# Performance work log

Hardware: AMD Instinct MI355X
Metric: run time of the kernel (lower is better)

## Reference

```python
import jax, jax.numpy as jnp
from jax import lax
import numpy as np

B, C_IN, IMG = 128, 3, 64
NH, D, K = 128, 256, 1024
BETA = 0.1        # beta buffer initialized to beta_start
BA_ITERS = 5
EPS = 1e-10


def _conv(x, w, b, stride, pad):
    y = lax.conv_general_dilated(x, w, (stride, stride), ((pad, pad), (pad, pad)),
                                 dimension_numbers=("NCHW", "OIHW", "NCHW"))
    return y + b[None, :, None, None]


def _convT(x, w, b):
    # PyTorch ConvTranspose2d(k=4, s=2, p=1); w: [Cin, Cout, 4, 4]
    wt = jnp.flip(w, (2, 3)).transpose(1, 0, 2, 3)  # -> [Cout, Cin, 4, 4]
    y = lax.conv_general_dilated(x, wt, (1, 1), ((2, 2), (2, 2)),
                                 lhs_dilation=(2, 2),
                                 dimension_numbers=("NCHW", "OIHW", "NCHW"))
    return y + b[None, :, None, None]


def _res(x, w1, b1, w2, b2):
    h = jax.nn.relu(_conv(x, w1, b1, 1, 1))
    h = _conv(h, w2, b2, 1, 1)
    return jax.nn.relu(h + x)


def setup_inputs() -> dict:
    key = jax.random.key(0)
    ks = iter(jax.random.split(key, 40))

    def w(shape):
        fan_in = int(np.prod(shape[1:]))
        return jax.random.normal(next(ks), shape, jnp.float32) / np.float32(np.sqrt(fan_in))

    z = lambda n: jnp.zeros((n,), jnp.float32)
    inp = {"x": jax.random.normal(next(ks), (B, C_IN, IMG, IMG), jnp.float32)}
    inp.update(
        ew1=w((NH, 3, 4, 4)), eb1=z(NH),
        ew2=w((2 * NH, NH, 4, 4)), eb2=z(2 * NH),
        ew3=w((D, 2 * NH, 3, 3)), eb3=z(D),
        er1aw=w((D, D, 3, 3)), er1ab=z(D), er1bw=w((D, D, 3, 3)), er1bb=z(D),
        er2aw=w((D, D, 3, 3)), er2ab=z(D), er2bw=w((D, D, 3, 3)), er2bb=z(D),
        codebook=jax.random.uniform(next(ks), (K, D), jnp.float32, -1.0 / K, 1.0 / K),
        pi=jnp.full((K,), 1.0 / K, jnp.float32),
        dr1aw=w((D, D, 3, 3)), dr1ab=z(D), dr1bw=w((D, D, 3, 3)), dr1bb=z(D),
        dr2aw=w((D, D, 3, 3)), dr2ab=z(D), dr2bw=w((D, D, 3, 3)), dr2bb=z(D),
        dw1=w((2 * NH, D, 3, 3)), db1=z(2 * NH),
        dwt2=w((2 * NH, NH, 4, 4)), dbt2=z(NH),
        dwt3=w((NH, 3, 4, 4)), dbt3=z(3),
    )
    return inp


def reference(x, ew1, eb1, ew2, eb2, ew3, eb3,
              er1aw, er1ab, er1bw, er1bb, er2aw, er2ab, er2bw, er2bb,
              codebook, pi,
              dr1aw, dr1ab, dr1bw, dr1bb, dr2aw, dr2ab, dr2bw, dr2bb,
              dw1, db1, dwt2, dbt2, dwt3, dbt3):
    # ---- encoder: [B,3,H,W] -> [B,D,H/4,W/4] ----
    h = jax.nn.relu(_conv(x, ew1, eb1, 2, 1))
    h = jax.nn.relu(_conv(h, ew2, eb2, 2, 1))
    h = jax.nn.relu(_conv(h, ew3, eb3, 1, 1))
    h = _res(h, er1aw, er1ab, er1bw, er1bb)
    z = _res(h, er2aw, er2ab, er2bw, er2bb)

    Bn, Dn, Hl, Wl = z.shape
    zf = z.transpose(0, 2, 3, 1).reshape(-1, Dn)  # [N, D]

    # squared euclidean distances [N, K]
    d = (jnp.sum(zf * zf, axis=1, keepdims=True)
         + jnp.sum(codebook * codebook, axis=1)
         - 2.0 * (zf @ codebook.T))

    # ---- Blahut-Arimoto iterations ----
    Q = pi
    for _ in range(BA_ITERS):
        logits = jnp.log(jnp.clip(Q, EPS)) - BETA * d  # [N, K]
        P = jax.nn.softmax(logits, axis=1)
        Q = jnp.clip(jnp.mean(P, axis=0), EPS)

    zq_soft = P @ codebook                              # [N, D]
    idx = jnp.argmax(P, axis=1)

    commit = 0.25 * jnp.mean((zf - lax.stop_gradient(zq_soft)) ** 2)
    cb_loss = jnp.mean((zq_soft - lax.stop_gradient(zf)) ** 2)
    ent = -jnp.sum(Q * jnp.log(jnp.clip(Q, EPS)))
    ent_loss = -0.01 * ent

    zq_hard = codebook[idx]
    zq = zq_soft + lax.stop_gradient(zq_hard - zq_soft)  # straight-through
    zq = zq.reshape(Bn, Hl, Wl, Dn).transpose(0, 3, 1, 2)

    # ---- decoder ----
    h = _res(zq, dr1aw, dr1ab, dr1bw, dr1bb)
    h = _res(h, dr2aw, dr2ab, dr2bw, dr2bb)
    h = jax.nn.relu(_conv(h, dw1, db1, 1, 1))
    h = jax.nn.relu(_convT(h, dwt2, dbt2))
    x_recon = _convT(h, dwt3, dbt3)
    return x_recon, commit, cb_loss, ent_loss
```

## Files before the change

### kernel.cpp

```cpp
#include <hip/hip_runtime.h>
#include <math.h>

#define NB   128
#define DC   256
#define SP   256
#define NROW 32768
#define KCB  1024
#define BETA_F 0.1f
#define EPSQ 1e-10f

typedef __attribute__((ext_vector_type(8))) short s16x8;
typedef __attribute__((ext_vector_type(4))) short s16x4;
typedef __attribute__((ext_vector_type(4))) float f32x4;

__device__ __forceinline__ short f2bf(float f) {
  unsigned u = __builtin_bit_cast(unsigned, f);
  unsigned r = (u + 0x7FFFu + ((u >> 16) & 1u)) >> 16;
  return (short)r;
}
__device__ __forceinline__ float bf2f(short s) {
  unsigned u = ((unsigned)(unsigned short)s) << 16;
  return __builtin_bit_cast(float, u);
}
__device__ __forceinline__ unsigned pack2(float a, float b) {
  return (unsigned)(unsigned short)f2bf(a) | ((unsigned)(unsigned short)f2bf(b) << 16);
}

__global__ void init0_kernel(short* __restrict__ zerob, unsigned* __restrict__ ticket)
{
  if (threadIdx.x < 8) zerob[threadIdx.x] = 0;
  if (threadIdx.x == 0) *ticket = 0u;
}

__global__ void w3t10_kernel(
    const float* __restrict__ w0, const float* __restrict__ w1,
    const float* __restrict__ w2, const float* __restrict__ w3,
    const float* __restrict__ w4, const float* __restrict__ w5,
    const float* __restrict__ w6, const float* __restrict__ w7,
    const float* __restrict__ w8, const float* __restrict__ w9,
    short* __restrict__ o)
{
  const float* ws[10] = {w0, w1, w2, w3, w4, w5, w6, w7, w8, w9};
  const float* w = ws[blockIdx.y];
  const int i = blockIdx.x * 256 + threadIdx.x;
  const int ci = i & 255, co = (i >> 8) & 255, j = i >> 16;
  o[(size_t)blockIdx.y * 589824 + i] = f2bf(w[((size_t)(co * 256 + ci)) * 9 + j]);
}
__global__ void w2t_kernel(const float* __restrict__ w, short* __restrict__ o)
{
  const int i = blockIdx.x * 256 + threadIdx.x;
  const int ci = i & 127, co = (i >> 7) & 255, j = i >> 15;
  o[i] = f2bf(w[((size_t)(co * 128 + ci)) * 16 + j]);
}
__global__ void wtt2_kernel(const float* __restrict__ w, short* __restrict__ o)
{
  const int i = blockIdx.x * 256 + threadIdx.x;
  const int ci = i & 255, co = (i >> 8) & 127, j = (i >> 15) & 3, p = i >> 17;
  const int po = p >> 1, pq = p & 1, a = j >> 1, b2 = j & 1;
  const int kh = (1 - po) + 2 * a, kw = (1 - pq) + 2 * b2;
  o[i] = f2bf(w[((size_t)(ci * 128 + co)) * 16 + kh * 4 + kw]);
}
__global__ void cbbf_kernel(const float* __restrict__ cb, short* __restrict__ o)
{
  const int i = blockIdx.x * 256 + threadIdx.x;
  o[i] = f2bf(cb[i]);
}
__global__ void cbt_kernel(const float* __restrict__ cb, short* __restrict__ o)
{
  const int i = blockIdx.x * 256 + threadIdx.x;
  const int d = i >> 10, k = i & 1023;
  o[i] = f2bf(cb[(size_t)k * 256 + d]);
}

__global__ __launch_bounds__(256) void conv1_kernel(
    const float* __restrict__ x, const float* __restrict__ w,
    const float* __restrict__ bias, short* __restrict__ out)
{
  __shared__ float li[3][34][34];
  const int tid = threadIdx.x;
  const int tile = blockIdx.x;
  const int b = blockIdx.y;
  const int qy = tile >> 1, qx = tile & 1;
  const int ihlo = qy * 32 - 1, iwlo = qx * 32 - 1;
  for (int ci = 0; ci < 3; ++ci)
    for (int s = tid; s < 1156; s += 256) {
      const int r = s / 34, c = s - r * 34;
      const int ih = ihlo + r, iw = iwlo + c;
      float v = 0.f;
      if ((unsigned)ih < 64u && (unsigned)iw < 64u)
        v = x[((size_t)(b * 3 + ci) * 64 + ih) * 64 + iw];
      li[ci][r][c] = v;
    }
  __syncthreads();

  const int wv = tid >> 6, l = tid & 63;
  const int co0 = 2 * l, co1 = 2 * l + 1;
  float w0[48], w1[48];
#pragma unroll
  for (int j = 0; j < 48; ++j) {
    w0[j] = w[(size_t)co0 * 48 + j];
    w1[j] = w[(size_t)co1 * 48 + j];
  }
  const float b0 = bias[co0], b1 = bias[co1];

  for (int pass = 0; pass < 64; ++pass) {
    const int pix = pass * 4 + wv;
    const int py = pix >> 4, px = pix & 15;
    float s0 = b0, s1 = b1;
#pragma unroll
    for (int ci = 0; ci < 3; ++ci)
#pragma unroll
      for (int kh = 0; kh < 4; ++kh)
#pragma unroll
        for (int kw = 0; kw < 4; ++kw) {
          const int j = ci * 16 + kh * 4 + kw;
          const float v = li[ci][2 * py + kh][2 * px + kw];
          s0 = fmaf(v, w0[j], s0);
          s1 = fmaf(v, w1[j], s1);
        }
    s0 = fmaxf(s0, 0.f);
    s1 = fmaxf(s1, 0.f);
    const int oh = qy * 16 + py, ow = qx * 16 + px;
    ((unsigned*)(out + ((size_t)b * 1024 + oh * 32 + ow) * 128))[l] = pack2(s0, s1);
  }
}

template<int MODE, int KIT, int AK, int KPN, int TS>
__global__ __launch_bounds__(256) void igemm_kernel(
    const short* __restrict__ Abuf, const short* __restrict__ Bw,
    const float* __restrict__ bias, const short* __restrict__ res,
    short* __restrict__ outb, float* __restrict__ outf32,
    float* __restrict__ sacc, const short* __restrict__ zerob)
{
  __shared__ __align__(16) short Alds[4][8192];
  __shared__ float red[4];
  const int tid = threadIdx.x;
  const int wv = tid >> 6, l = tid & 63;
  const int wm = wv >> 1, wn = wv & 1;
  const int lcol = l & 15, lk = l >> 4;
  const int m0 = blockIdx.x * 128;

  int ncol0 = 0, po = 0, pq = 0;
  const short* Bp = Bw;
  if constexpr (MODE == 3) {
    po = blockIdx.y >> 1; pq = blockIdx.y & 1;
    Bp += (size_t)blockIdx.y * 131072;
  } else {
    ncol0 = blockIdx.y * 128;
    Bp += (size_t)ncol0 * KPN;
  }

  const int cpos = l & 3;
  const int rl_[2] = { (wv * 2) * 16 + (l >> 2), (wv * 2 + 1) * 16 + (l >> 2) };
  const int cc_[2] = { cpos ^ ((rl_[0] >> 1) & 3), cpos ^ ((rl_[1] >> 1) & 3) };

  f32x4 acc[4][4];
#pragma unroll
  for (int i = 0; i < 4; ++i)
#pragma unroll
    for (int j = 0; j < 4; ++j) acc[i][j] = (f32x4){0.f, 0.f, 0.f, 0.f};

  const int aoff_base = lcol * 32 + ((lk ^ ((lcol >> 1) & 3)) * 8);

  auto STAGE = [&](int it, int bufc) {
    int jj, kk;
    if constexpr (MODE == 0 || MODE == 3) { jj = it >> 3; kk = it & 7; }
    else if constexpr (MODE == 2)         { jj = it >> 2; kk = it & 3; }
    else                                  { jj = 0; kk = it; }
    const int choff = kk * 32;
    (void)jj;
#pragma unroll
    for (int q = 0; q < 2; ++q) {
      const int rl = rl_[q], cc = cc_[q];
      const int m = m0 + rl;
      const short* srcA;
      if constexpr (MODE == 0) {
        const int q3 = jj / 3;
        const int ih = ((m >> 4) & 15) + q3 - 1, iw = (m & 15) + (jj - q3 * 3) - 1;
        const bool v = ((unsigned)ih < 16u) & ((unsigned)iw < 16u);
        srcA = v ? Abuf + (size_t)((m & ~255) + ih * 16 + iw) * AK + choff + cc * 8 : zerob;
      } else if constexpr (MODE == 2) {
        const int ih = 2 * ((m >> 4) & 15) + (jj >> 2) - 1, iw = 2 * (m & 15) + (jj & 3) - 1;
        const bool v = ((unsigned)ih < 32u) & ((unsigned)iw < 32u);
        srcA = v ? Abuf + (size_t)((m >> 8) * 1024 + ih * 32 + iw) * AK + choff + cc * 8 : zerob;
      } else if constexpr (MODE == 3) {
        const int ih = ((m >> 4) & 15) + po - (jj >> 1), iw = (m & 15) + pq - (jj & 1);
        const bool v = ((unsigned)ih < 16u) & ((unsigned)iw < 16u);
        srcA = v ? Abuf + (size_t)((m & ~255) + ih * 16 + iw) * AK + choff + cc * 8 : zerob;
      } else {
        srcA = Abuf + (size_t)m * AK + choff + cc * 8;
      }
      __builtin_amdgcn_global_load_lds(
          (const __attribute__((address_space(1))) void*)srcA,
          (__attribute__((address_space(3))) void*)(&Alds[bufc][(wv * 2 + q) * 512]),
          16, 0, 0);
      const short* srcB = Bp + (size_t)jj * TS + (size_t)rl * KPN + choff + cc * 8;
      __builtin_amdgcn_global_load_lds(
          (const __attribute__((address_space(1))) void*)srcB,
          (__attribute__((address_space(3))) void*)(&Alds[bufc][4096 + (wv * 2 + q) * 512]),
          16, 0, 0);
    }
  };

  auto COMPUTE = [&](int bufc) {
    s16x8 a[4], b[4];
#pragma unroll
    for (int ms = 0; ms < 4; ++ms)
      a[ms] = *(const s16x8*)&Alds[bufc][wm * 2048 + ms * 512 + aoff_base];
#pragma unroll
    for (int ns = 0; ns < 4; ++ns)
      b[ns] = *(const s16x8*)&Alds[bufc][4096 + wn * 2048 + ns * 512 + aoff_base];
#pragma unroll
    for (int ms = 0; ms < 4; ++ms)
#pragma unroll
      for (int ns = 0; ns < 4; ++ns)
        acc[ms][ns] = __builtin_amdgcn_mfma_f32_16x16x32_bf16(a[ms], b[ns], acc[ms][ns], 0, 0, 0);
  };

  STAGE(0, 0);
  STAGE(1, 1);
  STAGE(2, 2);
  int buf = 0, nbuf = 3;
#pragma unroll 1
  for (int it = 0; it < KIT; ++it) {
    if (it + 2 < KIT) {
      asm volatile("s_waitcnt vmcnt(8)" ::: "memory");
    } else if (it + 1 < KIT) {
      asm volatile("s_waitcnt vmcnt(4)" ::: "memory");
    } else {
      asm volatile("s_waitcnt vmcnt(0)" ::: "memory");
    }
    __builtin_amdgcn_s_barrier();
    if (it + 3 < KIT) STAGE(it + 3, nbuf);
    __builtin_amdgcn_s_setprio(1);
    COMPUTE(buf);
    __builtin_amdgcn_s_setprio(0);
    buf = (buf + 1) & 3;
    nbuf = (nbuf + 1) & 3;
  }

  const int r4 = lk * 4;
  float ls = 0.f;
#pragma unroll
  for (int ms = 0; ms < 4; ++ms) {
#pragma unroll
    for (int ns = 0; ns < 4; ++ns) {
      const int n_l = wn * 64 + ns * 16 + lcol;
      const int n_g = ncol0 + n_l;
#pragma unroll
      for (int e = 0; e < 4; ++e) {
        const int m = m0 + wm * 64 + ms * 16 + r4 + e;
        if constexpr (MODE == 4) {
          const float val = bias[n_g] - 2.f * acc[ms][ns][e];
          outb[(size_t)m * 1024 + n_g] = f2bf(val);
        } else if constexpr (MODE == 5) {
          const float d = acc[ms][ns][e] - outf32[(size_t)m * 256 + n_g];
          ls = fmaf(d, d, ls);
        } else if constexpr (MODE == 3) {
          const float val = fmaxf(acc[ms][ns][e] + bias[n_l], 0.f);
          const int orow = (m & ~255) * 4 + (2 * ((m >> 4) & 15) + po) * 32 + (2 * (m & 15) + pq);
          outb[(size_t)orow * 128 + n_l] = f2bf(val);
        } else {
          float val = acc[ms][ns][e] + bias[n_g];
          if (res) val += bf2f(res[(size_t)m * 256 + n_g]);
          val = fmaxf(val, 0.f);
          outb[(size_t)m * 256 + n_g] = f2bf(val);
          if (outf32) outf32[(size_t)m * 256 + n_g] = val;
        }
      }
    }
  }
  if constexpr (MODE == 5) {
#pragma unroll
    for (int o = 32; o > 0; o >>= 1) ls += __shfl_xor(ls, o);
    if (l == 0) red[wv] = ls;
    __syncthreads();
    if (tid == 0) atomicAdd(sacc, red[0] + red[1] + red[2] + red[3]);
  }
}

__global__ __launch_bounds__(256) void rownorm_kernel(
    const float* __restrict__ a, float* __restrict__ nrm, int rows)
{
  const int wv = threadIdx.x >> 6, lane = threadIdx.x & 63;
  const int r = blockIdx.x * 4 + wv;
  if (r >= rows) return;
  const float* p = a + (size_t)r * DC;
  float s = 0.f;
#pragma unroll
  for (int i = 0; i < 4; ++i) { float v = p[lane + 64 * i]; s = fmaf(v, v, s); }
#pragma unroll
  for (int o = 32; o > 0; o >>= 1) s += __shfl_xor(s, o);
  if (lane == 0) nrm[r] = s;
}

__global__ void initq_kernel(const float* __restrict__ pi, float* __restrict__ logq,
                             float* __restrict__ Sacc)
{
  const int k = blockIdx.x * 256 + threadIdx.x;
  logq[k] = logf(fmaxf(pi[k], EPSQ));
  if (k == 0) *Sacc = 0.f;
}

__global__ __launch_bounds__(256) void ba2_kernel(
    uint4* __restrict__ DV, const float* __restrict__ logq,
    float* __restrict__ part, int* __restrict__ idxout, int storeP)
{
  __shared__ float qp[4][1024];
  const int tid = threadIdx.x;
  const int wv = tid >> 6, lane = tid & 63;

  float lq[16];
  {
    const float4* lq4 = (const float4*)logq;
#pragma unroll
    for (int h = 0; h < 2; ++h) {
      const float4 a = lq4[h * 128 + 2 * lane];
      const float4 b = lq4[h * 128 + 2 * lane + 1];
      lq[h * 8 + 0] = a.x; lq[h * 8 + 1] = a.y; lq[h * 8 + 2] = a.z; lq[h * 8 + 3] = a.w;
      lq[h * 8 + 4] = b.x; lq[h * 8 + 5] = b.y; lq[h * 8 + 6] = b.z; lq[h * 8 + 7] = b.w;
    }
  }

  float qacc[16];
#pragma unroll
  for (int j = 0; j < 16; ++j) qacc[j] = 0.f;

  const int n0 = blockIdx.x * 16;
  for (int rr = 0; rr < 4; ++rr) {
    const int n = n0 + wv * 4 + rr;
    uint4* rowp = DV + (size_t)n * 128;
    uint4 w[2];
    w[0] = rowp[lane];
    w[1] = rowp[64 + lane];
    float lv[16];
    float mx = -1e30f;
#pragma unroll
    for (int h = 0; h < 2; ++h) {
      const unsigned* u = (const unsigned*)&w[h];
#pragma unroll
      for (int p = 0; p < 4; ++p) {
        lv[h * 8 + 2 * p]     = lq[h * 8 + 2 * p]     - BETA_F * bf2f((short)(u[p] & 0xFFFFu));
        lv[h * 8 + 2 * p + 1] = lq[h * 8 + 2 * p + 1] - BETA_F * bf2f((short)(u[p] >> 16));
      }
    }
#pragma unroll
    for (int j = 0; j < 16; ++j) mx = fmaxf(mx, lv[j]);
#pragma unroll
    for (int o = 32; o > 0; o >>= 1) mx = fmaxf(mx, __shfl_xor(mx, o));
    float e[16];
    float s = 0.f;
#pragma unroll
    for (int j = 0; j < 16; ++j) { e[j] = __expf(lv[j] - mx); s += e[j]; }
#pragma unroll
    for (int o = 32; o > 0; o >>= 1) s += __shfl_xor(s, o);
    const float inv = 1.f / s;
#pragma unroll
    for (int j = 0; j < 16; ++j) qacc[j] += e[j] * inv;

    if (storeP) {
#pragma unroll
      for (int h = 0; h < 2; ++h) {
        unsigned* u = (unsigned*)&w[h];
#pragma unroll
        for (int p = 0; p < 4; ++p)
          u[p] = pack2(e[h * 8 + 2 * p] * inv, e[h * 8 + 2 * p + 1] * inv);
      }
      rowp[lane] = w[0];
      rowp[64 + lane] = w[1];
      float bv = lv[0]; int bi = 8 * lane;
#pragma unroll
      for (int h = 0; h < 2; ++h)
#pragma unroll
        for (int j = 0; j < 8; ++j) {
          const int k = h * 512 + 8 * lane + j;
          const float v = lv[h * 8 + j];
          if (v > bv || (v == bv && k < bi)) { bv = v; bi = k; }
        }
#pragma unroll
      for (int o = 32; o > 0; o >>= 1) {
        const float ov = __shfl_xor(bv, o);
        const int oi = __shfl_xor(bi, o);
        if (ov > bv || (ov == bv && oi < bi)) { bv = ov; bi = oi; }
      }
      if (lane == 0) idxout[n] = bi;
    }
  }
  __syncthreads();
#pragma unroll
  for (int h = 0; h < 2; ++h)
#pragma unroll
    for (int j = 0; j < 8; ++j)
      qp[wv][h * 512 + 8 * lane + j] = qacc[h * 8 + j];
  __syncthreads();
  for (int k = tid; k < 1024; k += 256) {
    part[(size_t)blockIdx.x * 1024 + k] = qp[0][k] + qp[1][k] + qp[2][k] + qp[3][k];
  }
}

__global__ __launch_bounds__(256) void qredf_kernel(
    const float* __restrict__ part, float* __restrict__ part2,
    float* __restrict__ qsum, float* __restrict__ logq, unsigned* __restrict__ ticket)
{
  const int b = blockIdx.x;
  const int tid = threadIdx.x;
  const float* p = part + (size_t)b * 32 * 1024;
#pragma unroll
  for (int j = 0; j < 4; ++j) {
    const int k = tid + j * 256;
    float s = 0.f;
#pragma unroll
    for (int r = 0; r < 32; ++r) s += p[(size_t)r * 1024 + k];
    part2[(size_t)b * 1024 + k] = s;
  }
  __threadfence();
  __shared__ unsigned lastv;
  if (tid == 0) lastv = atomicAdd(ticket, 1u);
  __syncthreads();
  if (lastv == 63u) {
    __threadfence();
#pragma unroll
    for (int j = 0; j < 4; ++j) {
      const int k = tid + j * 256;
      float s = 0.f;
#pragma unroll
      for (int r = 0; r < 64; ++r) s += part2[(size_t)r * 1024 + k];
      qsum[k] = s;
      logq[k] = logf(fmaxf(s * (1.f / 32768.f), EPSQ));
    }
    if (tid == 0) *ticket = 0u;
  }
}

__global__ __launch_bounds__(1024) void entsc_kernel(
    const float* __restrict__ qsum, const float* __restrict__ S, float* __restrict__ out3)
{
  const int k = threadIdx.x;
  const float q = fmaxf(qsum[k] * (1.f / 32768.f), EPSQ);
  float v = q * logf(q);
#pragma unroll
  for (int o = 32; o > 0; o >>= 1) v += __shfl_xor(v, o);
  __shared__ float red[16];
  const int wv = k >> 6, lane = k & 63;
  if (lane == 0) red[wv] = v;
  __syncthreads();
  if (k == 0) {
    float s = 0.f;
    for (int i = 0; i < 16; ++i) s += red[i];
    out3[2] = 0.01f * s;
    const float sa = *S;
    out3[0] = 0.25f * sa / 8388608.f;
    out3[1] = sa / 8388608.f;
  }
}

__global__ void gather16_kernel(const int* __restrict__ idx, const short* __restrict__ cbb,
                                short* __restrict__ out)
{
  const int t = blockIdx.x * 256 + threadIdx.x;
  const int m = t >> 6, d4 = (t & 63) * 4;
  *(s16x4*)(out + (size_t)m * 256 + d4) = *(const s16x4*)(cbb + (size_t)idx[m] * 256 + d4);
}

__global__ __launch_bounds__(256) void convt3_kernel(
    const short* __restrict__ in, const float* __restrict__ w,
    const float* __restrict__ bias, float* __restrict__ out)
{
  __shared__ __align__(16) short li[100 * 128];
  __shared__ float lw[6144];
  const int tid = threadIdx.x;
  const int tile = blockIdx.x;
  const int b = blockIdx.y;
  const int ty0 = (tile >> 2) * 16, tx0 = (tile & 3) * 16;
  const int iy0 = (tile >> 2) * 8 - 1, ix0 = (tile & 3) * 8 - 1;
  for (int s = tid; s < 1600; s += 256) {
    const int pix = s >> 4, ch = s & 15;
    const int r = pix / 10, c = pix - r * 10;
    const int ih = iy0 + r, iw = ix0 + c;
    s16x8 v = {0, 0, 0, 0, 0, 0, 0, 0};
    if ((unsigned)ih < 32u && (unsigned)iw < 32u)
      v = *(const s16x8*)(in + ((size_t)b * 1024 + ih * 32 + iw) * 128 + ch * 8);
    const int slot = ch ^ (pix & 15);
    *(s16x8*)&li[pix * 128 + slot * 8] = v;
  }
  for (int s = tid; s < 6144; s += 256) lw[s] = w[s];
  __syncthreads();
  const int ty = tid >> 4, tx = tid & 15;
  const int oh2 = ty0 + ty, ow2 = tx0 + tx;
  const int kh0 = (oh2 + 1) & 1, kw0 = (ow2 + 1) & 1;
  const int ih0 = (oh2 + 1 - kh0) >> 1, iw0 = (ow2 + 1 - kw0) >> 1;
  const int rl0 = ih0 - iy0, cl0 = iw0 - ix0;
  const int p00 = rl0 * 10 + cl0, p01 = p00 - 1, p10 = p00 - 10, p11 = p00 - 11;
  const int wi00 = kh0 * 4 + kw0, wi01 = wi00 + 2, wi10 = wi00 + 8, wi11 = wi00 + 10;
  float acc0 = 0.f, acc1 = 0.f, acc2 = 0.f;
  for (int ch = 0; ch < 16; ++ch) {
    const s16x8 v00 = *(const s16x8*)&li[p00 * 128 + (ch ^ (p00 & 15)) * 8];
    const s16x8 v01 = *(const s16x8*)&li[p01 * 128 + (ch ^ (p01 & 15)) * 8];
    const s16x8 v10 = *(const s16x8*)&li[p10 * 128 + (ch ^ (p10 & 15)) * 8];
    const s16x8 v11 = *(const s16x8*)&li[p11 * 128 + (ch ^ (p11 & 15)) * 8];
#pragma unroll
    for (int e = 0; e < 8; ++e) {
      const int ci = ch * 8 + e;
      const float* wr = &lw[ci * 48];
      const float f00 = bf2f(v00[e]), f01 = bf2f(v01[e]);
      const float f10 = bf2f(v10[e]), f11 = bf2f(v11[e]);
      acc0 = fmaf(wr[wi00], f00, fmaf(wr[wi01], f01, fmaf(wr[wi10], f10, fmaf(wr[wi11], f11, acc0))));
      acc1 = fmaf(wr[16 + wi00], f00, fmaf(wr[16 + wi01], f01, fmaf(wr[16 + wi10], f10, fmaf(wr[16 + wi11], f11, acc1))));
      acc2 = fmaf(wr[32 + wi00], f00, fmaf(wr[32 + wi01], f01, fmaf(wr[32 + wi10], f10, fmaf(wr[32 + wi11], f11, acc2))));
    }
  }
  const size_t ob = ((size_t)(b * 3) * 64 + oh2) * 64 + ow2;
  out[ob] = acc0 + bias[0];
  out[ob + 4096] = acc1 + bias[1];
  out[ob + 8192] = acc2 + bias[2];
}

extern "C" void kernel_launch(void* const* d_in, const int* in_sizes, int n_in,
                              void* d_out, int out_size, void* d_ws, size_t ws_size,
                              hipStream_t stream)
{
  const float* x     = (const float*)d_in[0];
  const float* ew1   = (const float*)d_in[1];
  const float* eb1   = (const float*)d_in[2];
  const float* ew2   = (const float*)d_in[3];
  const float* eb2   = (const float*)d_in[4];
  const float* ew3   = (const float*)d_in[5];
  const float* eb3   = (const float*)d_in[6];
  const float* er1aw = (const float*)d_in[7];
  const float* er1ab = (const float*)d_in[8];
  const float* er1bw = (const float*)d_in[9];
  const float* er1bb = (const float*)d_in[10];
  const float* er2aw = (const float*)d_in[11];
  const float* er2ab = (const float*)d_in[12];
  const float* er2bw = (const float*)d_in[13];
  const float* er2bb = (const float*)d_in[14];
  const float* cb    = (const float*)d_in[15];
  const float* pi    = (const float*)d_in[16];
  const float* dr1aw = (const float*)d_in[17];
  const float* dr1ab = (const float*)d_in[18];
  const float* dr1bw = (const float*)d_in[19];
  const float* dr1bb = (const float*)d_in[20];
  const float* dr2aw = (const float*)d_in[21];
  const float* dr2ab = (const float*)d_in[22];
  const float* dr2bw = (const float*)d_in[23];
  const float* dr2bb = (const float*)d_in[24];
  const float* dw1   = (const float*)d_in[25];
  const float* db1   = (const float*)d_in[26];
  const float* dwt2  = (const float*)d_in[27];
  const float* dbt2  = (const float*)d_in[28];
  const float* dwt3  = (const float*)d_in[29];
  const float* dbt3  = (const float*)d_in[30];

  float* outf = (float*)d_out;

  char* W = (char*)d_ws;
  short* BIGA  = (short*)W;
  float* ZF32  = (float*)W;
  short* DV    = (short*)(W + 33554432);
  short* X0    = (short*)(W + 100663296);
  short* X1    = (short*)(W + 117440512);
  short* X2    = (short*)(W + 134217728);
  short* WT2   = (short*)(W + 152174592);
  short* WTT2  = (short*)(W + 153223168);
  short* CBB   = (short*)(W + 154271744);
  short* CBT   = (short*)(W + 154796032);
  float* cn    = (float*)(W + 155320320);
  float* qsum  = (float*)(W + 155324416);
  float* logq  = (float*)(W + 155328512);
  int*   idx   = (int*)(W + 155332608);
  float* Sacc  = (float*)(W + 155463680);
  short* zerob = (short*)(W + 155463696);
  unsigned* ticket = (unsigned*)(W + 155463712);
  float* PART  = (float*)(W + 160000000);
  float* PART2 = (float*)(W + 168388608);
  short* WT3S  = (short*)(W + 168650752);

  const dim3 blk(256);
  #define WTSLAB(i) (WT3S + (size_t)(i) * 589824)
  #define IG3(A_, Wi_, B_, R_, O_, F_) \
    igemm_kernel<0,72,256,256,65536><<<dim3(256, 2), blk, 0, stream>>>( \
        A_, WTSLAB(Wi_), B_, R_, O_, F_, nullptr, zerob)

  init0_kernel<<<dim3(1), dim3(64), 0, stream>>>(zerob, ticket);
  w3t10_kernel<<<dim3(2304, 10), blk, 0, stream>>>(
      ew3, er1aw, er1bw, er2aw, er2bw, dr1aw, dr1bw, dr2aw, dr2bw, dw1, WT3S);

  conv1_kernel<<<dim3(4, NB), blk, 0, stream>>>(x, ew1, eb1, BIGA);
  w2t_kernel<<<dim3(2048), blk, 0, stream>>>(ew2, WT2);
  igemm_kernel<2,64,128,128,32768><<<dim3(256, 2), blk, 0, stream>>>(
      BIGA, WT2, eb2, nullptr, X0, nullptr, nullptr, zerob);
  IG3(X0, 0, eb3, nullptr, X1, nullptr);
  IG3(X1, 1, er1ab, nullptr, X2, nullptr);
  IG3(X2, 2, er1bb, X1, X0, nullptr);
  IG3(X0, 3, er2ab, nullptr, X1, nullptr);
  IG3(X1, 4, er2bb, X0, X2, ZF32);

  rownorm_kernel<<<dim3(KCB / 4), blk, 0, stream>>>(cb, cn, KCB);
  cbbf_kernel<<<dim3(1024), blk, 0, stream>>>(cb, CBB);
  cbt_kernel<<<dim3(1024), blk, 0, stream>>>(cb, CBT);
  initq_kernel<<<dim3(4), blk, 0, stream>>>(pi, logq, Sacc);
  igemm_kernel<4,8,256,256,0><<<dim3(256, 8), blk, 0, stream>>>(
      X2, CBB, cn, nullptr, DV, nullptr, nullptr, zerob);
  for (int i = 0; i < 5; ++i) {
    ba2_kernel<<<dim3(NROW / 16), blk, 0, stream>>>(
        (uint4*)DV, logq, PART, idx, (i == 4) ? 1 : 0);
    qredf_kernel<<<dim3(64), blk, 0, stream>>>(PART, PART2, qsum, logq, ticket);
  }
  igemm_kernel<5,32,1024,1024,0><<<dim3(256, 2), blk, 0, stream>>>(
      DV, CBT, nullptr, nullptr, nullptr, ZF32, Sacc, zerob);
  entsc_kernel<<<dim3(1), dim3(1024), 0, stream>>>(qsum, Sacc, outf + 1572864);
  gather16_kernel<<<dim3(8192), blk, 0, stream>>>(idx, CBB, X0);

  IG3(X0, 5, dr1ab, nullptr, X1, nullptr);
  IG3(X1, 6, dr1bb, X0, X2, nullptr);
  IG3(X2, 7, dr2ab, nullptr, X0, nullptr);
  IG3(X0, 8, dr2bb, X2, X1, nullptr);
  IG3(X1, 9, db1, nullptr, X0, nullptr);
  wtt2_kernel<<<dim3(2048), blk, 0, stream>>>(dwt2, WTT2);
  igemm_kernel<3,32,256,256,32768><<<dim3(256, 4), blk, 0, stream>>>(
      X0, WTT2, dbt2, nullptr, BIGA, nullptr, nullptr, zerob);
  convt3_kernel<<<dim3(16, NB), blk, 0, stream>>>(BIGA, dwt3, dbt3, outf);
  #undef IG3
  #undef WTSLAB
}
```

Baseline: 949.0 us.

## Use 512-thread 128x256 tile GEMM kernel for non-transpose convolutions

Adds an 8-wave igemm variant whose block computes a 128x256 output tile, so each A tile staged in LDS is reused across all 256 output columns instead of being reloaded by two 128-column blocks. The grid halves in the N dimension and LDS per block grows to 96KB across four buffers. The old kernel is reduced to the transposed-conv mode only. This cuts redundant A-operand global traffic, but lowers the number of blocks and may reduce occupancy.

```diff
diff --git a/kernel.cpp b/kernel.cpp
--- a/kernel.cpp
+++ b/kernel.cpp
@@ -126,6 +126,152 @@
 }
 
 template<int MODE, int KIT, int AK, int KPN, int TS>
+__global__ __launch_bounds__(512) void igemm8_kernel(
+    const short* __restrict__ Abuf, const short* __restrict__ Bw,
+    const float* __restrict__ bias, const short* __restrict__ res,
+    short* __restrict__ outb, float* __restrict__ outf32,
+    float* __restrict__ sacc, const short* __restrict__ zerob)
+{
+  __shared__ __align__(16) short Alds[4][12288];
+  __shared__ float red[8];
+  const int tid = threadIdx.x;
+  const int wv = tid >> 6, l = tid & 63;
+  const int wm = wv >> 2, wn = wv & 3;
+  const int lcol = l & 15, lk = l >> 4;
+  const int m0 = blockIdx.x * 128;
+
+  const int ncol0 = blockIdx.y * 256;
+  const short* Bp = Bw + (size_t)ncol0 * KPN;
+
+  const int rlA = wv * 16 + (l >> 2);
+  const int ccA = (l & 3) ^ ((rlA >> 1) & 3);
+  const int colB_[2] = { wv * 32 + (l >> 2), wv * 32 + 16 + (l >> 2) };
+  const int ccB_[2] = { (l & 3) ^ ((colB_[0] >> 1) & 3), (l & 3) ^ ((colB_[1] >> 1) & 3) };
+
+  f32x4 acc[4][4];
+#pragma unroll
+  for (int i = 0; i < 4; ++i)
+#pragma unroll
+    for (int j = 0; j < 4; ++j) acc[i][j] = (f32x4){0.f, 0.f, 0.f, 0.f};
+
+  const int aoff_base = lcol * 32 + ((lk ^ ((lcol >> 1) & 3)) * 8);
+
+  auto STAGE = [&](int it, int bufc) {
+    int jj, kk;
+    if constexpr (MODE == 0)      { jj = it >> 3; kk = it & 7; }
+    else if constexpr (MODE == 2) { jj = it >> 2; kk = it & 3; }
+    else                          { jj = 0; kk = it; }
+    const int choff = kk * 32;
+    (void)jj;
+    {
+      const int m = m0 + rlA;
+      const short* srcA;
+      if constexpr (MODE == 0) {
+        const int q3 = jj / 3;
+        const int ih = ((m >> 4) & 15) + q3 - 1, iw = (m & 15) + (jj - q3 * 3) - 1;
+        const bool v = ((unsigned)ih < 16u) & ((unsigned)iw < 16u);
+        srcA = v ? Abuf + (size_t)((m & ~255) + ih * 16 + iw) * AK + choff + ccA * 8 : zerob;
+      } else if constexpr (MODE == 2) {
+        const int ih = 2 * ((m >> 4) & 15) + (jj >> 2) - 1, iw = 2 * (m & 15) + (jj & 3) - 1;
+        const bool v = ((unsigned)ih < 32u) & ((unsigned)iw < 32u);
+        srcA = v ? Abuf + (size_t)((m >> 8) * 1024 + ih * 32 + iw) * AK + choff + ccA * 8 : zerob;
+      } else {
+        srcA = Abuf + (size_t)m * AK + choff + ccA * 8;
+      }
+      __builtin_amdgcn_global_load_lds(
+          (const __attribute__((address_space(1))) void*)srcA,
+          (__attribute__((address_space(3))) void*)(&Alds[bufc][wv * 512]),
+          16, 0, 0);
+    }
+#pragma unroll
+    for (int q = 0; q < 2; ++q) {
+      const short* srcB = Bp + (size_t)jj * TS + (size_t)colB_[q] * KPN + choff + ccB_[q] * 8;
+      __builtin_amdgcn_global_load_lds(
+          (const __attribute__((address_space(1))) void*)srcB,
+          (__attribute__((address_space(3))) void*)(&Alds[bufc][4096 + wv * 1024 + q * 512]),
+          16, 0, 0);
+    }
+  };
+
+  auto COMPUTE = [&](int bufc) {
+    s16x8 a[4], b[4];
+#pragma unroll
+    for (int ms = 0; ms < 4; ++ms)
+      a[ms] = *(const s16x8*)&Alds[bufc][wm * 2048 + ms * 512 + aoff_base];
+#pragma unroll
+    for (int ns = 0; ns < 4; ++ns)
+      b[ns] = *(const s16x8*)&Alds[bufc][4096 + wn * 2048 + ns * 512 + aoff_base];
+#pragma unroll
+    for (int ms = 0; ms < 4; ++ms)
+#pragma unroll
+      for (int ns = 0; ns < 4; ++ns)
+        acc[ms][ns] = __builtin_amdgcn_mfma_f32_16x16x32_bf16(a[ms], b[ns], acc[ms][ns], 0, 0, 0);
+  };
+
+  STAGE(0, 0);
+  STAGE(1, 1);
+  STAGE(2, 2);
+  int buf = 0, nbuf = 3;
+#pragma unroll 1
+  for (int it = 0; it < KIT; ++it) {
+    if (it + 2 < KIT) {
+      asm volatile("s_waitcnt vmcnt(6)" ::: "memory");
+    } else if (it + 1 < KIT) {
+      asm volatile("s_waitcnt vmcnt(3)" ::: "memory");
+    } else {
+      asm volatile("s_waitcnt vmcnt(0)" ::: "memory");
+    }
+    __builtin_amdgcn_s_barrier();
+    if (it + 3 < KIT) STAGE(it + 3, nbuf);
+    __builtin_amdgcn_s_setprio(1);
+    COMPUTE(buf);
+    __builtin_amdgcn_s_setprio(0);
+    buf = (buf + 1) & 3;
+    nbuf = (nbuf + 1) & 3;
+  }
+
+  const int r4 = lk * 4;
+  float ls = 0.f;
+#pragma unroll
+  for (int ms = 0; ms < 4; ++ms) {
+#pragma unroll
+    for (int ns = 0; ns < 4; ++ns) {
+      const int n_l = wn * 64 + ns * 16 + lcol;
+      const int n_g = ncol0 + n_l;
+#pragma unroll
+      for (int e = 0; e < 4; ++e) {
+        const int m = m0 + wm * 64 + ms * 16 + r4 + e;
+        if constexpr (MODE == 4) {
+          const float val = bias[n_g] - 2.f * acc[ms][ns][e];
+          outb[(size_t)m * 1024 + n_g] = f2bf(val);
+        } else if constexpr (MODE == 5) {
+          const float d = acc[ms][ns][e] - outf32[(size_t)m * 256 + n_g];
+          ls = fmaf(d, d, ls);
+        } else {
+          float val = acc[ms][ns][e] + bias[n_g];
+          if (res) val += bf2f(res[(size_t)m * 256 + n_g]);
+          val = fmaxf(val, 0.f);
+          outb[(size_t)m * 256 + n_g] = f2bf(val);
+          if (outf32) outf32[(size_t)m * 256 + n_g] = val;
+        }
+      }
+    }
+  }
+  if constexpr (MODE == 5) {
+#pragma unroll
+    for (int o = 32; o > 0; o >>= 1) ls += __shfl_xor(ls, o);
+    if (l == 0) red[wv] = ls;
+    __syncthreads();
+    if (tid == 0) {
+      float s = 0.f;
+#pragma unroll
+      for (int i = 0; i < 8; ++i) s += red[i];
+      atomicAdd(sacc, s);
+    }
+  }
+}
+
+template<int MODE, int KIT, int AK, int KPN, int TS>
 __global__ __launch_bounds__(256) void igemm_kernel(
     const short* __restrict__ Abuf, const short* __restrict__ Bw,
     const float* __restrict__ bias, const short* __restrict__ res,
@@ -133,22 +279,14 @@
     float* __restrict__ sacc, const short* __restrict__ zerob)
 {
   __shared__ __align__(16) short Alds[4][8192];
-  __shared__ float red[4];
   const int tid = threadIdx.x;
   const int wv = tid >> 6, l = tid & 63;
   const int wm = wv >> 1, wn = wv & 1;
   const int lcol = l & 15, lk = l >> 4;
   const int m0 = blockIdx.x * 128;
 
-  int ncol0 = 0, po = 0, pq = 0;
-  const short* Bp = Bw;
-  if constexpr (MODE == 3) {
-    po = blockIdx.y >> 1; pq = blockIdx.y & 1;
-    Bp += (size_t)blockIdx.y * 131072;
-  } else {
-    ncol0 = blockIdx.y * 128;
-    Bp += (size_t)ncol0 * KPN;
-  }
+  const int po = blockIdx.y >> 1, pq = blockIdx.y & 1;
+  const short* Bp = Bw + (size_t)blockIdx.y * 131072;
 
   const int cpos = l & 3;
   const int rl_[2] = { (wv * 2) * 16 + (l >> 2), (wv * 2 + 1) * 16 + (l >> 2) };
@@ -163,33 +301,15 @@
   const int aoff_base = lcol * 32 + ((lk ^ ((lcol >> 1) & 3)) * 8);
 
   auto STAGE = [&](int it, int bufc) {
-    int jj, kk;
-    if constexpr (MODE == 0 || MODE == 3) { jj = it >> 3; kk = it & 7; }
-    else if constexpr (MODE == 2)         { jj = it >> 2; kk = it & 3; }
-    else                                  { jj = 0; kk = it; }
+    const int jj = it >> 3, kk = it & 7;
     const int choff = kk * 32;
-    (void)jj;
 #pragma unroll
     for (int q = 0; q < 2; ++q) {
       const int rl = rl_[q], cc = cc_[q];
       const int m = m0 + rl;
-      const short* srcA;
-      if constexpr (MODE == 0) {
-        const int q3 = jj / 3;
-        const int ih = ((m >> 4) & 15) + q3 - 1, iw = (m & 15) + (jj - q3 * 3) - 1;
-        const bool v = ((unsigned)ih < 16u) & ((unsigned)iw < 16u);
-        srcA = v ? Abuf + (size_t)((m & ~255) + ih * 16 + iw) * AK + choff + cc * 8 : zerob;
-      } else if constexpr (MODE == 2) {
-        const int ih = 2 * ((m >> 4) & 15) + (jj >> 2) - 1, iw = 2 * (m & 15) + (jj & 3) - 1;
-        const bool v = ((unsigned)ih < 32u) & ((unsigned)iw < 32u);
-        srcA = v ? Abuf + (size_t)((m >> 8) * 1024 + ih * 32 + iw) * AK + choff + cc * 8 : zerob;
-      } else if constexpr (MODE == 3) {
-        const int ih = ((m >> 4) & 15) + po - (jj >> 1), iw = (m & 15) + pq - (jj & 1);
-        const bool v = ((unsigned)ih < 16u) & ((unsigned)iw < 16u);
-        srcA = v ? Abuf + (size_t)((m & ~255) + ih * 16 + iw) * AK + choff + cc * 8 : zerob;
-      } else {
-        srcA = Abuf + (size_t)m * AK + choff + cc * 8;
-      }
+      const int ih = ((m >> 4) & 15) + po - (jj >> 1), iw = (m & 15) + pq - (jj & 1);
+      const bool v = ((unsigned)ih < 16u) & ((unsigned)iw < 16u);
+      const short* srcA = v ? Abuf + (size_t)((m & ~255) + ih * 16 + iw) * AK + choff + cc * 8 : zerob;
       __builtin_amdgcn_global_load_lds(
           (const __attribute__((address_space(1))) void*)srcA,
           (__attribute__((address_space(3))) void*)(&Alds[bufc][(wv * 2 + q) * 512]),
@@ -240,42 +360,19 @@
   }
 
   const int r4 = lk * 4;
-  float ls = 0.f;
 #pragma unroll
   for (int ms = 0; ms < 4; ++ms) {
 #pragma unroll
     for (int ns = 0; ns < 4; ++ns) {
       const int n_l = wn * 64 + ns * 16 + lcol;
-      const int n_g = ncol0 + n_l;
 #pragma unroll
       for (int e = 0; e < 4; ++e) {
         const int m = m0 + wm * 64 + ms * 16 + r4 + e;
-        if constexpr (MODE == 4) {
-          const float val = bias[n_g] - 2.f * acc[ms][ns][e];
-          outb[(size_t)m * 1024 + n_g] = f2bf(val);
-        } else if constexpr (MODE == 5) {
-          const float d = acc[ms][ns][e] - outf32[(size_t)m * 256 + n_g];
-          ls = fmaf(d, d, ls);
-        } else if constexpr (MODE == 3) {
-          const float val = fmaxf(acc[ms][ns][e] + bias[n_l], 0.f);
-          const int orow = (m & ~255) * 4 + (2 * ((m >> 4) & 15) + po) * 32 + (2 * (m & 15) + pq);
-          outb[(size_t)orow * 128 + n_l] = f2bf(val);
-        } else {
-          float val = acc[ms][ns][e] + bias[n_g];
-          if (res) val += bf2f(res[(size_t)m * 256 + n_g]);
-          val = fmaxf(val, 0.f);
-          outb[(size_t)m * 256 + n_g] = f2bf(val);
-          if (outf32) outf32[(size_t)m * 256 + n_g] = val;
-        }
+        const float val = fmaxf(acc[ms][ns][e] + bias[n_l], 0.f);
+        const int orow = (m & ~255) * 4 + (2 * ((m >> 4) & 15) + po) * 32 + (2 * (m & 15) + pq);
+        outb[(size_t)orow * 128 + n_l] = f2bf(val);
       }
     }
-  }
-  if constexpr (MODE == 5) {
-#pragma unroll
-    for (int o = 32; o > 0; o >>= 1) ls += __shfl_xor(ls, o);
-    if (l == 0) red[wv] = ls;
-    __syncthreads();
-    if (tid == 0) atomicAdd(sacc, red[0] + red[1] + red[2] + red[3]);
   }
 }
 
@@ -576,9 +673,10 @@
   short* WT3S  = (short*)(W + 168650752);
 
   const dim3 blk(256);
+  const dim3 blk8(512);
   #define WTSLAB(i) (WT3S + (size_t)(i) * 589824)
   #define IG3(A_, Wi_, B_, R_, O_, F_) \
-    igemm_kernel<0,72,256,256,65536><<<dim3(256, 2), blk, 0, stream>>>( \
+    igemm8_kernel<0,72,256,256,65536><<<dim3(256), blk8, 0, stream>>>( \
         A_, WTSLAB(Wi_), B_, R_, O_, F_, nullptr, zerob)
 
   init0_kernel<<<dim3(1), dim3(64), 0, stream>>>(zerob, ticket);
@@ -587,7 +685,7 @@
 
   conv1_kernel<<<dim3(4, NB), blk, 0, stream>>>(x, ew1, eb1, BIGA);
   w2t_kernel<<<dim3(2048), blk, 0, stream>>>(ew2, WT2);
-  igemm_kernel<2,64,128,128,32768><<<dim3(256, 2), blk, 0, stream>>>(
+  igemm8_kernel<2,64,128,128,32768><<<dim3(256), blk8, 0, stream>>>(
       BIGA, WT2, eb2, nullptr, X0, nullptr, nullptr, zerob);
   IG3(X0, 0, eb3, nullptr, X1, nullptr);
   IG3(X1, 1, er1ab, nullptr, X2, nullptr);
@@ -599,14 +697,14 @@
   cbbf_kernel<<<dim3(1024), blk, 0, stream>>>(cb, CBB);
   cbt_kernel<<<dim3(1024), blk, 0, stream>>>(cb, CBT);
   initq_kernel<<<dim3(4), blk, 0, stream>>>(pi, logq, Sacc);
-  igemm_kernel<4,8,256,256,0><<<dim3(256, 8), blk, 0, stream>>>(
+  igemm8_kernel<4,8,256,256,0><<<dim3(256, 4), blk8, 0, stream>>>(
       X2, CBB, cn, nullptr, DV, nullptr, nullptr, zerob);
   for (int i = 0; i < 5; ++i) {
     ba2_kernel<<<dim3(NROW / 16), blk, 0, stream>>>(
         (uint4*)DV, logq, PART, idx, (i == 4) ? 1 : 0);
     qredf_kernel<<<dim3(64), blk, 0, stream>>>(PART, PART2, qsum, logq, ticket);
   }
-  igemm_kernel<5,32,1024,1024,0><<<dim3(256, 2), blk, 0, stream>>>(
+  igemm8_kernel<5,32,1024,1024,0><<<dim3(256), blk8, 0, stream>>>(
       DV, CBT, nullptr, nullptr, nullptr, ZF32, Sacc, zerob);
   entsc_kernel<<<dim3(1), dim3(1024), 0, stream>>>(qsum, Sacc, outf + 1572864);
   gather16_kernel<<<dim3(8192), blk, 0, stream>>>(idx, CBB, X0);
```

Result: no change. 959.9 us (+1.1%).
